# Performance work log

Hardware: AMD Instinct MI355X
Metric: run time of the kernel (lower is better)

Reference implementation:

```python
import jax, jax.numpy as jnp
import numpy as np

B, T, E = 256, 33, 1024
L = T - 1  # one distinct LSTM per timestep


def setup_inputs() -> dict:
    key = jax.random.key(0)
    k1, k2, k3, k4 = jax.random.split(key, 4)
    scale = 1.0 / np.sqrt(E)  # matches nn.LSTM default uniform init
    return {
        "input_feature_vectors": jax.random.normal(k1, (B, T, E), jnp.float32),
        "target_feature_vector": jax.random.normal(k2, (B, E), jnp.float32),
        "W_ih": jax.random.uniform(k3, (L, 4 * E, E), jnp.float32, -scale, scale),
        "W_hh": jax.random.uniform(k4, (L, 4 * E, E), jnp.float32, -scale, scale),
    }


def _lstm_step(carry, inp):
    h, c = carry                      # [B, E] each
    x_t, w_ih, w_hh = inp             # [B, E], [4E, E], [4E, E]
    gates = x_t @ w_ih.T + h @ w_hh.T  # [B, 4E]; bias=False in the original
    i, f, g, o = jnp.split(gates, 4, axis=-1)  # torch gate order: i, f, g, o
    i = jax.nn.sigmoid(i)
    f = jax.nn.sigmoid(f)
    g = jnp.tanh(g)
    o = jax.nn.sigmoid(o)
    c = f * c + i * g
    h = o * jnp.tanh(c)
    return (h, c), None


def reference(input_feature_vectors, target_feature_vector, W_ih, W_hh):
    x = input_feature_vectors
    b, t, e = x.shape
    h0 = jnp.zeros((b, e), x.dtype)            # h_0 = zeros(1, B, E)
    c0 = x[:, 1, :]                            # c_0 = input[:, 1:2, :].transpose(0,1)
    xs = jnp.swapaxes(x[:, : t - 1, :], 0, 1)  # [T-1, B, E], steps 0..T-2
    (h, c), _ = jax.lax.scan(_lstm_step, (h0, c0), (xs, W_ih, W_hh))
    # output[:, 0, :] of the last step is the final h
    loss = jnp.mean(jnp.abs(h - target_feature_vector))  # L1Loss (mean)
    return loss, h, c
```

## Files before the change

### kernel.cpp

```cpp
#include <hip/hip_runtime.h>
#include <hip/hip_bf16.h>

typedef __attribute__((ext_vector_type(8))) short bf16x8;
typedef __attribute__((ext_vector_type(4))) float f32x4;
typedef __attribute__((ext_vector_type(16))) float f32x16;

static constexpr int BB = 256;
static constexpr int TT = 33;
static constexpr int EE = 1024;
static constexpr int LL = 32;
static constexpr int NG = 4096;

static constexpr int BUF_SZ  = 24576;
static constexpr int A_OFF   = 16384;
static constexpr int NBUF    = 6;
static constexpr int LDS_DYN = 147456;

__device__ __forceinline__ short f2bf(float f) {
  unsigned u = __builtin_bit_cast(unsigned, f);
  u += 0x7fffu + ((u >> 16) & 1u);
  return (short)(u >> 16);
}

__device__ __forceinline__ bf16x8 cvt8(f32x4 a, f32x4 b) {
  bf16x8 r;
  r[0] = f2bf(a[0]); r[1] = f2bf(a[1]); r[2] = f2bf(a[2]); r[3] = f2bf(a[3]);
  r[4] = f2bf(b[0]); r[5] = f2bf(b[1]); r[6] = f2bf(b[2]); r[7] = f2bf(b[3]);
  return r;
}

__device__ __forceinline__ float sigm(float x) { return 1.0f / (1.0f + __expf(-x)); }
__device__ __forceinline__ float tanh_f(float x) { return 1.0f - 2.0f / (__expf(2.0f * x) + 1.0f); }

__global__ __launch_bounds__(256) void lstm_prep(
    const float* __restrict__ x, short* __restrict__ xbf, float* __restrict__ c_io,
    unsigned* __restrict__ flags)
{
  if (blockIdx.x == 0) flags[(size_t)threadIdx.x * 64] = 0;
  int gth = blockIdx.x * 256 + threadIdx.x;
  int eb  = gth & 127;
  int row = (gth >> 7) & 255;
  int t   = gth >> 15;
  const float* src = x + ((size_t)row * TT + t) * EE + (eb << 3);
  f32x4 lo = *(const f32x4*)src;
  f32x4 hi = *(const f32x4*)(src + 4);
  *(bf16x8*)(xbf + ((size_t)t * BB + row) * EE + (eb << 3)) = cvt8(lo, hi);
  if (t == 1) {
    float* cd = c_io + (size_t)row * EE + (eb << 3);
    *(f32x4*)cd = lo;
    *(f32x4*)(cd + 4) = hi;
  }
}

__global__ __launch_bounds__(512) void lstm_rec(
    const short* __restrict__ xbf,
    const float* __restrict__ Wih,
    const float* __restrict__ Whh,
    short* __restrict__ hroll,
    float* __restrict__ c_io,
    float* __restrict__ h_out,
    unsigned* __restrict__ flags)
{
  extern __shared__ __align__(16) char smem[];

  const int tid  = threadIdx.x;
  const int lane = tid & 63;
  const int wv   = tid >> 6;
  const int ct   = wv & 1;
  const int kh   = wv >> 1;

  const int wg     = blockIdx.x;
  const int xcd    = wg & 7;
  const int jj     = wg >> 3;
  const int rowgrp = jj & 3;
  const int ehi    = jj >> 2;
  const int e0     = (xcd * 8 + ehi) << 4;
  const int row0   = rowgrp << 6;

  size_t wsrc_off[2]; int wdst_off[2];
#pragma unroll
  for (int r = 0; r < 2; ++r) {
    int o = r * 8192 + wv * 1024 + lane * 16;
    int lrow = o >> 8;
    int mwr = ((lrow & 7) << 5) | ((lrow & 8) << 1);
    wsrc_off[r] = (size_t)((lrow >> 4) * EE + e0 + (lrow & 15)) * 4096 + ((o & 255) ^ mwr);
    wdst_off[r] = r * 8192 + wv * 1024;
  }
  size_t asrc_off; int adst_off;
  {
    int o  = wv * 1024 + lane * 16;
    int G  = o >> 4;
    int rp = G >> 4;
    int s  = G & 15;
    int r  = rp * 2 + (s & 1);
    int g  = ((s >> 1) ^ (rp & 7)) & 7;
    asrc_off = (size_t)(row0 + r) * 2048 + g * 16;
    adst_off = A_OFF + o;
  }

  const int wrow    = ct * 32 + (lane & 31);
  const int mwr2    = ((wrow & 7) << 5) | ((wrow & 8) << 1);
  const int kW      = kh * 64 + ((lane >> 5) << 5);
  const int woff_lo = wrow * 256 + (kW ^ mwr2);
  const int woff_hi = wrow * 256 + ((kW + 16) ^ mwr2);
  const int arow    = lane & 31;
  const int rpA     = arow >> 1;
  const int gkh     = kh * 2 + (lane >> 5);
  const int sA      = (2 * gkh + (arow & 1)) ^ ((rpA & 7) << 1);
  const int aoff0   = rpA * 256 + sA * 16;

  const int er  = tid & 63;
  const int ee_ = tid >> 6;
  float c0r = c_io[(size_t)(row0 + er) * EE + e0 + ee_];
  float c1r = c_io[(size_t)(row0 + er) * EE + e0 + ee_ + 8];

  f32x16 acc0{}, acc1{};

  auto stageC = [&](int tt, int cc, int buf) {
    const int p  = cc >> 4;
    const int k0 = (cc & 15) << 6;
    const char* Wt = (const char*)((p ? Whh : Wih) + (size_t)tt * NG * EE);
    const char* At = p ? (const char*)(hroll + (size_t)(tt - 1) * BB * EE)
                       : (const char*)(xbf + (size_t)tt * BB * EE);
    char* dst = smem + buf * BUF_SZ;
#pragma unroll
    for (int r = 0; r < 2; ++r)
      __builtin_amdgcn_global_load_lds(
          (const __attribute__((address_space(1))) unsigned int*)(Wt + wsrc_off[r] + (k0 << 2)),
          (__attribute__((address_space(3))) unsigned int*)(dst + wdst_off[r]), 16, 0, 0);
    __builtin_amdgcn_global_load_lds(
        (const __attribute__((address_space(1))) unsigned int*)(At + asrc_off + (k0 << 1)),
        (__attribute__((address_space(3))) unsigned int*)(dst + adst_off), 16, 0, 0);
  };

  auto compute = [&](int buf) {
    const char* Wb = smem + buf * BUF_SZ;
    const char* Ab = Wb + A_OFF;
    f32x4 wlo = *(const f32x4*)(Wb + woff_lo);
    f32x4 whi = *(const f32x4*)(Wb + woff_hi);
    bf16x8 bfr = cvt8(wlo, whi);
    bf16x8 a0 = *(const bf16x8*)(Ab + aoff0);
    bf16x8 a1 = *(const bf16x8*)(Ab + aoff0 + 4096);
    acc0 = __builtin_amdgcn_mfma_f32_32x32x16_bf16(a0, bfr, acc0, 0, 0, 0);
    acc1 = __builtin_amdgcn_mfma_f32_32x32x16_bf16(a1, bfr, acc1, 0, 0, 0);
  };

  const int rsw = ((lane >> 1) & 3) << 4;
  auto dumpT = [&](float* base, const f32x16& a) {
    char* b = (char*)base + lane * 64;
#pragma unroll
    for (int jq = 0; jq < 4; ++jq) {
      f32x4 v{a[jq * 4 + 0], a[jq * 4 + 1], a[jq * 4 + 2], a[jq * 4 + 3]};
      *(f32x4*)(b + ((jq * 16) ^ rsw)) = v;
    }
  };
  auto addT = [&](const float* base, f32x16& a) {
    const char* b = (const char*)base + lane * 64;
#pragma unroll
    for (int jq = 0; jq < 4; ++jq) {
      f32x4 v = *(const f32x4*)(b + ((jq * 16) ^ rsw));
      a[jq * 4 + 0] += v[0]; a[jq * 4 + 1] += v[1];
      a[jq * 4 + 2] += v[2]; a[jq * 4 + 3] += v[3];
    }
  };

  stageC(0, 0, 0); stageC(0, 1, 1); stageC(0, 2, 2); stageC(0, 3, 3);

  int fb = 0;
  for (int t = 0; t < LL; ++t) {
    const int nch = t ? 32 : 16;
    for (int pc = 0; pc < nch / 2; ++pc) {
      if (t == LL - 1 && pc == nch / 2 - 1) asm volatile("s_waitcnt vmcnt(0)" ::: "memory");
      else                                   asm volatile("s_waitcnt vmcnt(6)" ::: "memory");
      __builtin_amdgcn_s_barrier();
      compute(fb);
      compute((fb + 1) % NBUF);

      int sc0 = 2 * pc + 4, st = t;
      if (sc0 >= nch) { sc0 -= nch; st = t + 1; }
      bool skip = (st > t && sc0 == 2) || (st >= LL);
      if (!skip) {
        if (st == t && sc0 == 16) {
          if (tid < 256) {
            while (__hip_atomic_load(flags + (size_t)tid * 64,
                                     __ATOMIC_RELAXED, __HIP_MEMORY_SCOPE_AGENT) < (unsigned)t)
              __builtin_amdgcn_s_sleep(1);
          }
          __builtin_amdgcn_s_barrier();
          __builtin_amdgcn_sched_barrier(0);
        }
        stageC(st, sc0,     (fb + 4) % NBUF);
        stageC(st, sc0 + 1, (fb + 5) % NBUF);
      }
      fb = (fb + 2) % NBUF;
    }

    float* red  = (float*)(smem + (size_t)((fb + 4) % NBUF) * BUF_SZ);
    char*  glsb = smem + (size_t)((fb + 5) % NBUF) * BUF_SZ;
    auto slotp = [&](int src, int rt) { return red + (size_t)((ct * 2 + src) * 2 + rt) * 1024; };

    if (kh >= 2) { dumpT(slotp(kh - 2, 0), acc0); dumpT(slotp(kh - 2, 1), acc1); }
    asm volatile("s_waitcnt lgkmcnt(0)" ::: "memory");
    __builtin_amdgcn_s_barrier();
    if (kh < 2) { addT(slotp(kh, 0), acc0); addT(slotp(kh, 1), acc1); }
    asm volatile("s_waitcnt lgkmcnt(0)" ::: "memory");
    __builtin_amdgcn_s_barrier();
    if (kh == 1) { dumpT(slotp(0, 0), acc0); dumpT(slotp(0, 1), acc1); }
    asm volatile("s_waitcnt lgkmcnt(0)" ::: "memory");
    __builtin_amdgcn_s_barrier();
    if (kh == 0) {
      addT(slotp(0, 0), acc0);
      addT(slotp(0, 1), acc1);
      char* gb = glsb + wrow * 256;
#pragma unroll
      for (int rt = 0; rt < 2; ++rt) {
        const f32x16& a = rt ? acc1 : acc0;
#pragma unroll
        for (int jq = 0; jq < 4; ++jq) {
          int rowb = rt * 128 + jq * 32 + ((lane >> 5) << 4);
          f32x4 v{a[jq * 4 + 0], a[jq * 4 + 1], a[jq * 4 + 2], a[jq * 4 + 3]};
          *(f32x4*)(gb + (rowb ^ mwr2)) = v;
        }
      }
    }
    acc0 = f32x16{}; acc1 = f32x16{};
    asm volatile("s_waitcnt lgkmcnt(0)" ::: "memory");
    __builtin_amdgcn_s_barrier();

    {
      short* hh = (short*)(glsb + 16384);
      auto gate = [&](int g, int ee) {
        int wc = g * 16 + ee;
        int swc = ((wc & 7) << 5) | ((wc & 8) << 1);
        return *(const float*)(glsb + wc * 256 + ((er * 4) ^ swc));
      };
      float gi0 = gate(0, ee_), gf0 = gate(1, ee_), gg0 = gate(2, ee_), go0 = gate(3, ee_);
      float gi1 = gate(0, ee_ + 8), gf1 = gate(1, ee_ + 8), gg1 = gate(2, ee_ + 8), go1 = gate(3, ee_ + 8);

      c0r = sigm(gf0) * c0r + sigm(gi0) * tanh_f(gg0);
      float h0n = sigm(go0) * tanh_f(c0r);
      c1r = sigm(gf1) * c1r + sigm(gi1) * tanh_f(gg1);
      float h1n = sigm(go1) * tanh_f(c1r);

      hh[er * 16 + ee_]     = f2bf(h0n);
      hh[er * 16 + ee_ + 8] = f2bf(h1n);

      if (t == LL - 1) {
        size_t o0 = (size_t)(row0 + er) * EE + e0 + ee_;
        size_t o1 = o0 + 8;
        h_out[o0] = h0n; c_io[o0] = c0r;
        h_out[o1] = h1n; c_io[o1] = c1r;
      }
    }
    asm volatile("s_waitcnt lgkmcnt(0)" ::: "memory");
    __builtin_amdgcn_s_barrier();

    if (t < LL - 1) {
      if (tid < 256) {
        int r = tid >> 2, q = tid & 3;
        unsigned long long v = *(const unsigned long long*)(glsb + 16384 + r * 32 + q * 8);
        __hip_atomic_store(
            (unsigned long long*)((char*)hroll + ((size_t)t * BB + row0 + r) * 2048 + (size_t)e0 * 2 + q * 8),
            v, __ATOMIC_RELAXED, __HIP_MEMORY_SCOPE_AGENT);
      }
      stageC(t + 1, 2, (fb + 2) % NBUF);
      stageC(t + 1, 3, (fb + 3) % NBUF);
      asm volatile("s_waitcnt vmcnt(6)" ::: "memory");
      __builtin_amdgcn_s_barrier();
      if (tid == 0)
        __hip_atomic_store(flags + (size_t)wg * 64, (unsigned)(t + 1),
                           __ATOMIC_RELAXED, __HIP_MEMORY_SCOPE_AGENT);
    }
  }
}

__global__ __launch_bounds__(256) void lstm_loss_part(
    const float* __restrict__ h, const float* __restrict__ tgt, float* __restrict__ partials)
{
  __shared__ float lds[4];
  int tid = threadIdx.x;
  float s = 0.f;
  int base = blockIdx.x * 1024 + tid;
#pragma unroll
  for (int q = 0; q < 4; ++q) {
    int idx = base + (q << 8);
    s += fabsf(h[idx] - tgt[idx]);
  }
#pragma unroll
  for (int off = 32; off > 0; off >>= 1) s += __shfl_down(s, off, 64);
  if ((tid & 63) == 0) lds[tid >> 6] = s;
  __syncthreads();
  if (tid == 0) partials[blockIdx.x] = lds[0] + lds[1] + lds[2] + lds[3];
}

__global__ __launch_bounds__(256) void lstm_loss_fin(
    const float* __restrict__ partials, float* __restrict__ out)
{
  __shared__ float lds[4];
  int tid = threadIdx.x;
  float s = partials[tid];
#pragma unroll
  for (int off = 32; off > 0; off >>= 1) s += __shfl_down(s, off, 64);
  if ((tid & 63) == 0) lds[tid >> 6] = s;
  __syncthreads();
  if (tid == 0) out[0] = (lds[0] + lds[1] + lds[2] + lds[3]) * (1.0f / 262144.0f);
}

extern "C" void kernel_launch(void* const* d_in, const int* in_sizes, int n_in,
                              void* d_out, int out_size, void* d_ws, size_t ws_size,
                              hipStream_t stream) {
  const float* x   = (const float*)d_in[0];
  const float* tgt = (const float*)d_in[1];
  const float* Wih = (const float*)d_in[2];
  const float* Whh = (const float*)d_in[3];

  float* out   = (float*)d_out;
  float* h_out = out + 1;
  float* c_io  = out + 1 + BB * EE;

  short* xbf      = (short*)d_ws;
  short* hroll    = (short*)((char*)xbf + (size_t)LL * BB * EE * 2);
  float* partials = (float*)((char*)hroll + (size_t)LL * BB * EE * 2);
  unsigned* flags = (unsigned*)((char*)partials + 1024);

  static bool attr_done = false;
  if (!attr_done) {
    hipFuncSetAttribute((const void*)lstm_rec,
                        hipFuncAttributeMaxDynamicSharedMemorySize, LDS_DYN);
    attr_done = true;
  }

  lstm_prep<<<4096, 256, 0, stream>>>(x, xbf, c_io, flags);

  {
    const short* xbfA = xbf; const float* WihA = Wih; const float* WhhA = Whh;
    short* hrollA = hroll; float* cA = c_io; float* hA = h_out; unsigned* flagsA = flags;
    void* args[] = {&xbfA, &WihA, &WhhA, &hrollA, &cA, &hA, &flagsA};
    hipError_t e = hipLaunchCooperativeKernel((void*)lstm_rec, dim3(256), dim3(512),
                                              args, LDS_DYN, stream);
    if (e != hipSuccess)
      lstm_rec<<<256, 512, LDS_DYN, stream>>>(xbf, Wih, Whh, hroll, c_io, h_out, flags);
  }

  lstm_loss_part<<<256, 256, 0, stream>>>(h_out, tgt, partials);
  lstm_loss_fin<<<1, 256, 0, stream>>>(partials, out);
}
```

Before: 542.8 us.

## Load fp32 weights into registers and store bf16 to LDS, halving buffer size

Weight tiles were copied to LDS as fp32 through global_load_lds, and every wave converted them to bf16 at compute time. Now each thread loads its slice of fp32 weights into registers one phase ahead, converts once, and writes bf16 into a smaller LDS buffer (16KB instead of 24KB per stage), which cuts LDS footprint and removes the redundant per-wave conversion. The pipeline is restructured into ping-pong register phases with adjusted vmcnt waits, and the reduction/gate scratch is folded into one buffer. This adds register pressure and VGPR-path global loads that may be less efficient than the direct-to-LDS copies, and it makes the wait-count bookkeeping more fragile.

```diff
diff --git a/kernel.cpp b/kernel.cpp
--- a/kernel.cpp
+++ b/kernel.cpp
@@ -11,10 +11,10 @@
 static constexpr int LL = 32;
 static constexpr int NG = 4096;
 
-static constexpr int BUF_SZ  = 24576;
-static constexpr int A_OFF   = 16384;
+static constexpr int BUF_SZ  = 16384;
+static constexpr int A_OFF   = 8192;
 static constexpr int NBUF    = 6;
-static constexpr int LDS_DYN = 147456;
+static constexpr int LDS_DYN = 98304;
 
 __device__ __forceinline__ short f2bf(float f) {
   unsigned u = __builtin_bit_cast(unsigned, f);
@@ -77,15 +77,11 @@
   const int e0     = (xcd * 8 + ehi) << 4;
   const int row0   = rowgrp << 6;
 
-  size_t wsrc_off[2]; int wdst_off[2];
-#pragma unroll
-  for (int r = 0; r < 2; ++r) {
-    int o = r * 8192 + wv * 1024 + lane * 16;
-    int lrow = o >> 8;
-    int mwr = ((lrow & 7) << 5) | ((lrow & 8) << 1);
-    wsrc_off[r] = (size_t)((lrow >> 4) * EE + e0 + (lrow & 15)) * 4096 + ((o & 255) ^ mwr);
-    wdst_off[r] = r * 8192 + wv * 1024;
-  }
+  const int wr_  = tid >> 3;
+  const size_t wsrc2 = (size_t)((wr_ >> 4) * EE + e0 + (wr_ & 15)) * 4096 + (size_t)(tid & 7) * 32;
+  const int wdst2 = (wr_ >> 1) * 256
+                  + (((2 * (tid & 7) + (wr_ & 1)) ^ (((wr_ >> 1) & 7) << 1)) << 4);
+
   size_t asrc_off; int adst_off;
   {
     int o  = wv * 1024 + lane * 16;
@@ -98,16 +94,15 @@
     adst_off = A_OFF + o;
   }
 
-  const int wrow    = ct * 32 + (lane & 31);
-  const int mwr2    = ((wrow & 7) << 5) | ((wrow & 8) << 1);
-  const int kW      = kh * 64 + ((lane >> 5) << 5);
-  const int woff_lo = wrow * 256 + (kW ^ mwr2);
-  const int woff_hi = wrow * 256 + ((kW + 16) ^ mwr2);
-  const int arow    = lane & 31;
-  const int rpA     = arow >> 1;
-  const int gkh     = kh * 2 + (lane >> 5);
-  const int sA      = (2 * gkh + (arow & 1)) ^ ((rpA & 7) << 1);
-  const int aoff0   = rpA * 256 + sA * 16;
+  const int wrow = ct * 32 + (lane & 31);
+  const int mg   = ((wrow & 7) << 5) | ((wrow & 8) << 1);
+  const int g2   = kh * 2 + (lane >> 5);
+  const int wrd2 = (wrow >> 1) * 256
+                 + (((2 * g2 + (wrow & 1)) ^ (((wrow >> 1) & 7) << 1)) << 4);
+  const int arow = lane & 31;
+  const int rpA  = arow >> 1;
+  const int sA   = (2 * g2 + (arow & 1)) ^ ((rpA & 7) << 1);
+  const int aoff0 = rpA * 256 + sA * 16;
 
   const int er  = tid & 63;
   const int ee_ = tid >> 6;
@@ -115,34 +110,38 @@
   float c1r = c_io[(size_t)(row0 + er) * EE + e0 + ee_ + 8];
 
   f32x16 acc0{}, acc1{};
-
-  auto stageC = [&](int tt, int cc, int buf) {
+  int fb = 0;
+
+  auto stageA = [&](int tt, int cc, int buf) {
     const int p  = cc >> 4;
     const int k0 = (cc & 15) << 6;
-    const char* Wt = (const char*)((p ? Whh : Wih) + (size_t)tt * NG * EE);
     const char* At = p ? (const char*)(hroll + (size_t)(tt - 1) * BB * EE)
                        : (const char*)(xbf + (size_t)tt * BB * EE);
-    char* dst = smem + buf * BUF_SZ;
-#pragma unroll
-    for (int r = 0; r < 2; ++r)
-      __builtin_amdgcn_global_load_lds(
-          (const __attribute__((address_space(1))) unsigned int*)(Wt + wsrc_off[r] + (k0 << 2)),
-          (__attribute__((address_space(3))) unsigned int*)(dst + wdst_off[r]), 16, 0, 0);
     __builtin_amdgcn_global_load_lds(
         (const __attribute__((address_space(1))) unsigned int*)(At + asrc_off + (k0 << 1)),
-        (__attribute__((address_space(3))) unsigned int*)(dst + adst_off), 16, 0, 0);
+        (__attribute__((address_space(3))) unsigned int*)(smem + buf * BUF_SZ + adst_off), 16, 0, 0);
+  };
+
+  auto loadW = [&](int tt, int cc, f32x4& lo, f32x4& hi) {
+    const int p  = cc >> 4;
+    const int k0 = (cc & 15) << 6;
+    const float* Wt = (p ? Whh : Wih) + (size_t)tt * NG * EE;
+    const char* src = (const char*)Wt + wsrc2 + ((size_t)k0 << 2);
+    lo = *(const f32x4*)src;
+    hi = *(const f32x4*)(src + 16);
+  };
+
+  auto writeW = [&](const f32x4& lo, const f32x4& hi, int buf) {
+    *(bf16x8*)(smem + buf * BUF_SZ + wdst2) = cvt8(lo, hi);
   };
 
   auto compute = [&](int buf) {
-    const char* Wb = smem + buf * BUF_SZ;
-    const char* Ab = Wb + A_OFF;
-    f32x4 wlo = *(const f32x4*)(Wb + woff_lo);
-    f32x4 whi = *(const f32x4*)(Wb + woff_hi);
-    bf16x8 bfr = cvt8(wlo, whi);
-    bf16x8 a0 = *(const bf16x8*)(Ab + aoff0);
-    bf16x8 a1 = *(const bf16x8*)(Ab + aoff0 + 4096);
-    acc0 = __builtin_amdgcn_mfma_f32_32x32x16_bf16(a0, bfr, acc0, 0, 0, 0);
-    acc1 = __builtin_amdgcn_mfma_f32_32x32x16_bf16(a1, bfr, acc1, 0, 0, 0);
+    const char* Bb = smem + buf * BUF_SZ;
+    bf16x8 w  = *(const bf16x8*)(Bb + wrd2);
+    bf16x8 a0 = *(const bf16x8*)(Bb + A_OFF + aoff0);
+    bf16x8 a1 = *(const bf16x8*)(Bb + A_OFF + aoff0 + 4096);
+    acc0 = __builtin_amdgcn_mfma_f32_32x32x16_bf16(a0, w, acc0, 0, 0, 0);
+    acc1 = __builtin_amdgcn_mfma_f32_32x32x16_bf16(a1, w, acc1, 0, 0, 0);
   };
 
   const int rsw = ((lane >> 1) & 3) << 4;
@@ -164,40 +163,60 @@
     }
   };
 
-  stageC(0, 0, 0); stageC(0, 1, 1); stageC(0, 2, 2); stageC(0, 3, 3);
-
-  int fb = 0;
+  auto phase = [&](int c0, int t, int nch, int wc,
+                   f32x4& l0, f32x4& l1, f32x4& l2, f32x4& l3,
+                   f32x4& w0, f32x4& w1, f32x4& w2, f32x4& w3) {
+    if (wc) asm volatile("s_waitcnt vmcnt(6) lgkmcnt(0)" ::: "memory");
+    else    asm volatile("s_waitcnt vmcnt(0) lgkmcnt(0)" ::: "memory");
+    __builtin_amdgcn_s_barrier();
+    compute(fb);
+    compute(fb + 1);
+    int b2 = fb + 2 >= NBUF ? fb + 2 - NBUF : fb + 2;
+    int b3 = b2 + 1;
+    int b4 = b2 + 2 >= NBUF ? b2 + 2 - NBUF : b2 + 2;
+    int b5 = b4 + 1;
+    int sc2 = c0 + 4, st2 = t;  if (sc2 >= nch) { sc2 -= nch; st2 = t + 1; }
+    int sc1 = c0 + 2, st1 = t;  if (sc1 >= nch) { sc1 -= nch; st1 = t + 1; }
+    if (st2 < LL && !(st2 > t && sc2 == 2)) {
+      if (st2 == t && sc2 == 16) {
+        if (tid < 256) {
+          while (__hip_atomic_load(flags + (size_t)tid * 64,
+                                   __ATOMIC_RELAXED, __HIP_MEMORY_SCOPE_AGENT) < (unsigned)t)
+            __builtin_amdgcn_s_sleep(1);
+        }
+        __builtin_amdgcn_s_barrier();
+        __builtin_amdgcn_sched_barrier(0);
+      }
+      stageA(st2, sc2, b4);
+      stageA(st2, sc2 + 1, b5);
+    }
+    if (st2 < LL) { loadW(st2, sc2, l0, l1); loadW(st2, sc2 + 1, l2, l3); }
+    asm volatile("s_waitcnt vmcnt(6)" ::: "memory");
+    if (st1 < LL) { writeW(w0, w1, b2); writeW(w2, w3, b3); }
+    fb = b2;
+  };
+
+  stageA(0, 0, 0); stageA(0, 1, 1); stageA(0, 2, 2); stageA(0, 3, 3);
+  f32x4 A0{}, A1{}, A2{}, A3{}, B0{}, B1{}, B2{}, B3{};
+  loadW(0, 0, A0, A1); loadW(0, 1, A2, A3);
+  writeW(A0, A1, 0); writeW(A2, A3, 1);
+  loadW(0, 2, B0, B1); loadW(0, 3, B2, B3);
+
   for (int t = 0; t < LL; ++t) {
     const int nch = t ? 32 : 16;
-    for (int pc = 0; pc < nch / 2; ++pc) {
-      if (t == LL - 1 && pc == nch / 2 - 1) asm volatile("s_waitcnt vmcnt(0)" ::: "memory");
-      else                                   asm volatile("s_waitcnt vmcnt(6)" ::: "memory");
-      __builtin_amdgcn_s_barrier();
-      compute(fb);
-      compute((fb + 1) % NBUF);
-
-      int sc0 = 2 * pc + 4, st = t;
-      if (sc0 >= nch) { sc0 -= nch; st = t + 1; }
-      bool skip = (st > t && sc0 == 2) || (st >= LL);
-      if (!skip) {
-        if (st == t && sc0 == 16) {
-          if (tid < 256) {
-            while (__hip_atomic_load(flags + (size_t)tid * 64,
-                                     __ATOMIC_RELAXED, __HIP_MEMORY_SCOPE_AGENT) < (unsigned)t)
-              __builtin_amdgcn_s_sleep(1);
-          }
-          __builtin_amdgcn_s_barrier();
-          __builtin_amdgcn_sched_barrier(0);
-        }
-        stageC(st, sc0,     (fb + 4) % NBUF);
-        stageC(st, sc0 + 1, (fb + 5) % NBUF);
-      }
-      fb = (fb + 2) % NBUF;
-    }
-
-    float* red  = (float*)(smem + (size_t)((fb + 4) % NBUF) * BUF_SZ);
-    char*  glsb = smem + (size_t)((fb + 5) % NBUF) * BUF_SZ;
-    auto slotp = [&](int src, int rt) { return red + (size_t)((ct * 2 + src) * 2 + rt) * 1024; };
+    for (int c0 = 0; c0 < nch; c0 += 4) {
+      int wcA = !(t == LL - 1 && c0 + 4 >= nch);
+      int wcB = !(t == LL - 1 && c0 + 6 >= nch);
+      phase(c0,     t, nch, wcA, A0, A1, A2, A3, B0, B1, B2, B3);
+      phase(c0 + 2, t, nch, wcB, B0, B1, B2, B3, A0, A1, A2, A3);
+    }
+
+    asm volatile("s_waitcnt lgkmcnt(0)" ::: "memory");
+    __builtin_amdgcn_s_barrier();
+    char* red = smem + (size_t)((fb + 4) % NBUF) * BUF_SZ;
+    auto slotp = [&](int src, int rt) {
+      return (float*)(red + (size_t)((ct * 2 + src) * 2 + rt) * 4096);
+    };
 
     if (kh >= 2) { dumpT(slotp(kh - 2, 0), acc0); dumpT(slotp(kh - 2, 1), acc1); }
     asm volatile("s_waitcnt lgkmcnt(0)" ::: "memory");
@@ -211,7 +230,7 @@
     if (kh == 0) {
       addT(slotp(0, 0), acc0);
       addT(slotp(0, 1), acc1);
-      char* gb = glsb + wrow * 256;
+      char* gb = red + wrow * 256;
 #pragma unroll
       for (int rt = 0; rt < 2; ++rt) {
         const f32x16& a = rt ? acc1 : acc0;
@@ -219,7 +238,7 @@
         for (int jq = 0; jq < 4; ++jq) {
           int rowb = rt * 128 + jq * 32 + ((lane >> 5) << 4);
           f32x4 v{a[jq * 4 + 0], a[jq * 4 + 1], a[jq * 4 + 2], a[jq * 4 + 3]};
-          *(f32x4*)(gb + (rowb ^ mwr2)) = v;
+          *(f32x4*)(gb + (rowb ^ mg)) = v;
         }
       }
     }
@@ -228,11 +247,11 @@
     __builtin_amdgcn_s_barrier();
 
     {
-      short* hh = (short*)(glsb + 16384);
+      short* hh = (short*)(red + 16384);
       auto gate = [&](int g, int ee) {
         int wc = g * 16 + ee;
         int swc = ((wc & 7) << 5) | ((wc & 8) << 1);
-        return *(const float*)(glsb + wc * 256 + ((er * 4) ^ swc));
+        return *(const float*)(red + wc * 256 + ((er * 4) ^ swc));
       };
       float gi0 = gate(0, ee_), gf0 = gate(1, ee_), gg0 = gate(2, ee_), go0 = gate(3, ee_);
       float gi1 = gate(0, ee_ + 8), gf1 = gate(1, ee_ + 8), gg1 = gate(2, ee_ + 8), go1 = gate(3, ee_ + 8);
@@ -258,14 +277,14 @@
     if (t < LL - 1) {
       if (tid < 256) {
         int r = tid >> 2, q = tid & 3;
-        unsigned long long v = *(const unsigned long long*)(glsb + 16384 + r * 32 + q * 8);
+        unsigned long long v = *(const unsigned long long*)(red + 16384 + r * 32 + q * 8);
         __hip_atomic_store(
             (unsigned long long*)((char*)hroll + ((size_t)t * BB + row0 + r) * 2048 + (size_t)e0 * 2 + q * 8),
             v, __ATOMIC_RELAXED, __HIP_MEMORY_SCOPE_AGENT);
       }
-      stageC(t + 1, 2, (fb + 2) % NBUF);
-      stageC(t + 1, 3, (fb + 3) % NBUF);
-      asm volatile("s_waitcnt vmcnt(6)" ::: "memory");
+      stageA(t + 1, 2, (fb + 2) % NBUF);
+      stageA(t + 1, 3, (fb + 3) % NBUF);
+      asm volatile("s_waitcnt vmcnt(2)" ::: "memory");
       __builtin_amdgcn_s_barrier();
       if (tid == 0)
         __hip_atomic_store(flags + (size_t)wg * 64, (unsigned)(t + 1),
```

After: 816.5 us. +50.4%, slower.

## Restructure LSTM step epilogue: single-pass k-reduction, direct h stores, narrower flag wait

Applied to the files above, without the earlier changes.

Issues the next stage loads before the MFMA compute in each pipeline iteration, so loads overlap compute. The cross-wave k-split reduction drops from three barrier rounds to one: waves 1-3 dump their partial tiles and wave 0 sums all three. Each thread now owns two adjacent output columns and writes packed bf16 h directly to global memory, removing the LDS staging and one barrier. The flag wait now polls only the 64 producer flags relevant to this row group instead of all 256. This changes the buffer layout and dependency handling, which risks subtle ordering bugs, for example the extra vmcnt(0) wait added at pc==1.

```diff
diff --git a/kernel.cpp b/kernel.cpp
--- a/kernel.cpp
+++ b/kernel.cpp
@@ -98,21 +98,21 @@
     adst_off = A_OFF + o;
   }
 
-  const int wrow    = ct * 32 + (lane & 31);
-  const int mwr2    = ((wrow & 7) << 5) | ((wrow & 8) << 1);
-  const int kW      = kh * 64 + ((lane >> 5) << 5);
-  const int woff_lo = wrow * 256 + (kW ^ mwr2);
-  const int woff_hi = wrow * 256 + ((kW + 16) ^ mwr2);
-  const int arow    = lane & 31;
-  const int rpA     = arow >> 1;
-  const int gkh     = kh * 2 + (lane >> 5);
-  const int sA      = (2 * gkh + (arow & 1)) ^ ((rpA & 7) << 1);
-  const int aoff0   = rpA * 256 + sA * 16;
-
-  const int er  = tid & 63;
-  const int ee_ = tid >> 6;
-  float c0r = c_io[(size_t)(row0 + er) * EE + e0 + ee_];
-  float c1r = c_io[(size_t)(row0 + er) * EE + e0 + ee_ + 8];
+  const int wrow = ct * 32 + (lane & 31);
+  const int mg   = ((wrow & 7) << 5) | ((wrow & 8) << 1);
+  const int kW   = kh * 64 + ((lane >> 5) << 5);
+  const int woff_lo = wrow * 256 + (kW ^ mg);
+  const int woff_hi = wrow * 256 + ((kW + 16) ^ mg);
+  const int arow = lane & 31;
+  const int rpA  = arow >> 1;
+  const int gkh  = kh * 2 + (lane >> 5);
+  const int sA   = (2 * gkh + (arow & 1)) ^ ((rpA & 7) << 1);
+  const int aoff0 = rpA * 256 + sA * 16;
+
+  const int er = tid & 63;
+  const int ep = tid >> 6;
+  float c0r = c_io[(size_t)(row0 + er) * EE + e0 + 2 * ep];
+  float c1r = c_io[(size_t)(row0 + er) * EE + e0 + 2 * ep + 1];
 
   f32x16 acc0{}, acc1{};
 
@@ -169,20 +169,21 @@
   int fb = 0;
   for (int t = 0; t < LL; ++t) {
     const int nch = t ? 32 : 16;
-    for (int pc = 0; pc < nch / 2; ++pc) {
-      if (t == LL - 1 && pc == nch / 2 - 1) asm volatile("s_waitcnt vmcnt(0)" ::: "memory");
-      else                                   asm volatile("s_waitcnt vmcnt(6)" ::: "memory");
+    const int np  = nch >> 1;
+    for (int pc = 0; pc < np; ++pc) {
+      bool full = (t > 0 && pc == 1) || (t == LL - 1 && pc == np - 1);
+      if (full) asm volatile("s_waitcnt vmcnt(0)" ::: "memory");
+      else      asm volatile("s_waitcnt vmcnt(6)" ::: "memory");
       __builtin_amdgcn_s_barrier();
-      compute(fb);
-      compute((fb + 1) % NBUF);
 
       int sc0 = 2 * pc + 4, st = t;
       if (sc0 >= nch) { sc0 -= nch; st = t + 1; }
       bool skip = (st > t && sc0 == 2) || (st >= LL);
       if (!skip) {
         if (st == t && sc0 == 16) {
-          if (tid < 256) {
-            while (__hip_atomic_load(flags + (size_t)tid * 64,
+          if (tid < 64) {
+            unsigned fid = (unsigned)((tid & 7) + 8 * rowgrp + 32 * (tid >> 3));
+            while (__hip_atomic_load(flags + (size_t)fid * 64,
                                      __ATOMIC_RELAXED, __HIP_MEMORY_SCOPE_AGENT) < (unsigned)t)
               __builtin_amdgcn_s_sleep(1);
           }
@@ -192,26 +193,26 @@
         stageC(st, sc0,     (fb + 4) % NBUF);
         stageC(st, sc0 + 1, (fb + 5) % NBUF);
       }
+
+      compute(fb);
+      compute(fb + 1);
       fb = (fb + 2) % NBUF;
     }
 
-    float* red  = (float*)(smem + (size_t)((fb + 4) % NBUF) * BUF_SZ);
-    char*  glsb = smem + (size_t)((fb + 5) % NBUF) * BUF_SZ;
-    auto slotp = [&](int src, int rt) { return red + (size_t)((ct * 2 + src) * 2 + rt) * 1024; };
-
-    if (kh >= 2) { dumpT(slotp(kh - 2, 0), acc0); dumpT(slotp(kh - 2, 1), acc1); }
+    __builtin_amdgcn_s_barrier();
+    char* red = smem + (size_t)((fb + 4) % NBUF) * BUF_SZ;
+    auto slotp = [&](int src, int rt) {
+      return (float*)(red + (size_t)((src * 2 + ct) * 2 + rt) * 4096);
+    };
+
+    if (kh >= 1) { dumpT(slotp(kh - 1, 0), acc0); dumpT(slotp(kh - 1, 1), acc1); }
     asm volatile("s_waitcnt lgkmcnt(0)" ::: "memory");
     __builtin_amdgcn_s_barrier();
-    if (kh < 2) { addT(slotp(kh, 0), acc0); addT(slotp(kh, 1), acc1); }
-    asm volatile("s_waitcnt lgkmcnt(0)" ::: "memory");
-    __builtin_amdgcn_s_barrier();
-    if (kh == 1) { dumpT(slotp(0, 0), acc0); dumpT(slotp(0, 1), acc1); }
-    asm volatile("s_waitcnt lgkmcnt(0)" ::: "memory");
-    __builtin_amdgcn_s_barrier();
+
     if (kh == 0) {
-      addT(slotp(0, 0), acc0);
-      addT(slotp(0, 1), acc1);
-      char* gb = glsb + wrow * 256;
+#pragma unroll
+      for (int src = 0; src < 3; ++src) { addT(slotp(src, 0), acc0); addT(slotp(src, 1), acc1); }
+      char* gb = red + wrow * 256;
 #pragma unroll
       for (int rt = 0; rt < 2; ++rt) {
         const f32x16& a = rt ? acc1 : acc0;
@@ -219,7 +220,7 @@
         for (int jq = 0; jq < 4; ++jq) {
           int rowb = rt * 128 + jq * 32 + ((lane >> 5) << 4);
           f32x4 v{a[jq * 4 + 0], a[jq * 4 + 1], a[jq * 4 + 2], a[jq * 4 + 3]};
-          *(f32x4*)(gb + (rowb ^ mwr2)) = v;
+          *(f32x4*)(gb + (rowb ^ mg)) = v;
         }
       }
     }
@@ -228,41 +229,34 @@
     __builtin_amdgcn_s_barrier();
 
     {
-      short* hh = (short*)(glsb + 16384);
       auto gate = [&](int g, int ee) {
         int wc = g * 16 + ee;
         int swc = ((wc & 7) << 5) | ((wc & 8) << 1);
-        return *(const float*)(glsb + wc * 256 + ((er * 4) ^ swc));
+        return *(const float*)(red + wc * 256 + ((er * 4) ^ swc));
       };
-      float gi0 = gate(0, ee_), gf0 = gate(1, ee_), gg0 = gate(2, ee_), go0 = gate(3, ee_);
-      float gi1 = gate(0, ee_ + 8), gf1 = gate(1, ee_ + 8), gg1 = gate(2, ee_ + 8), go1 = gate(3, ee_ + 8);
+      int e0c = 2 * ep;
+      float gi0 = gate(0, e0c), gf0 = gate(1, e0c), gg0 = gate(2, e0c), go0 = gate(3, e0c);
+      float gi1 = gate(0, e0c + 1), gf1 = gate(1, e0c + 1), gg1 = gate(2, e0c + 1), go1 = gate(3, e0c + 1);
 
       c0r = sigm(gf0) * c0r + sigm(gi0) * tanh_f(gg0);
       float h0n = sigm(go0) * tanh_f(c0r);
       c1r = sigm(gf1) * c1r + sigm(gi1) * tanh_f(gg1);
       float h1n = sigm(go1) * tanh_f(c1r);
 
-      hh[er * 16 + ee_]     = f2bf(h0n);
-      hh[er * 16 + ee_ + 8] = f2bf(h1n);
-
       if (t == LL - 1) {
-        size_t o0 = (size_t)(row0 + er) * EE + e0 + ee_;
-        size_t o1 = o0 + 8;
-        h_out[o0] = h0n; c_io[o0] = c0r;
-        h_out[o1] = h1n; c_io[o1] = c1r;
+        size_t o0 = (size_t)(row0 + er) * EE + e0 + e0c;
+        h_out[o0] = h0n;     c_io[o0] = c0r;
+        h_out[o0 + 1] = h1n; c_io[o0 + 1] = c1r;
+      } else {
+        unsigned pv = (unsigned)(unsigned short)f2bf(h0n)
+                    | ((unsigned)(unsigned short)f2bf(h1n) << 16);
+        __hip_atomic_store(
+            (unsigned*)((char*)hroll + ((size_t)t * BB + row0 + er) * 2048 + (size_t)(e0 + e0c) * 2),
+            pv, __ATOMIC_RELAXED, __HIP_MEMORY_SCOPE_AGENT);
       }
     }
-    asm volatile("s_waitcnt lgkmcnt(0)" ::: "memory");
-    __builtin_amdgcn_s_barrier();
 
     if (t < LL - 1) {
-      if (tid < 256) {
-        int r = tid >> 2, q = tid & 3;
-        unsigned long long v = *(const unsigned long long*)(glsb + 16384 + r * 32 + q * 8);
-        __hip_atomic_store(
-            (unsigned long long*)((char*)hroll + ((size_t)t * BB + row0 + r) * 2048 + (size_t)e0 * 2 + q * 8),
-            v, __ATOMIC_RELAXED, __HIP_MEMORY_SCOPE_AGENT);
-      }
       stageC(t + 1, 2, (fb + 2) % NBUF);
       stageC(t + 1, 3, (fb + 3) % NBUF);
       asm volatile("s_waitcnt vmcnt(6)" ::: "memory");
```

After: 593.3 us. +9.3%, slower.
